# Kernel optimization log

Hardware: AMD Instinct MI355X
Metric: run time of the kernel (lower is better)

Reference implementation:

```python
import jax, jax.numpy as jnp
import numpy as np

D_MODEL = 1024
H = 16
D_K = D_MODEL // H
D_FF = 4096
EPS = 1e-6
NEG = -1e9


def layer_norm(x, alpha, beta):
    # Custom LN: scalar alpha/beta, unbiased std, eps added to std (not var)
    mean = jnp.mean(x, axis=-1, keepdims=True)
    std = jnp.std(x, axis=-1, ddof=1, keepdims=True)
    return alpha * (x - mean) / (std + EPS) + beta


def setup_inputs() -> dict:
    key = jax.random.key(0)
    ks = jax.random.split(key, 16)
    B, S = 4, 2048
    s = 1.0 / np.sqrt(D_MODEL)
    inp = {
        "x": jax.random.normal(ks[0], (B, S, D_MODEL), dtype=jnp.float32),
        "src_mask": jax.random.randint(ks[1], (B, 1, 1, S), 0, 2, dtype=jnp.int32),
        "wq": jax.random.normal(ks[2], (D_MODEL, D_MODEL), jnp.float32) * s,
        "bq": jnp.zeros((D_MODEL,), jnp.float32),
        "wk": jax.random.normal(ks[3], (D_MODEL, D_MODEL), jnp.float32) * s,
        "bk": jnp.zeros((D_MODEL,), jnp.float32),
        "wv": jax.random.normal(ks[4], (D_MODEL, D_MODEL), jnp.float32) * s,
        "bv": jnp.zeros((D_MODEL,), jnp.float32),
        "wo": jax.random.normal(ks[5], (D_MODEL, D_MODEL), jnp.float32) * s,
        "bo": jnp.zeros((D_MODEL,), jnp.float32),
        "w1": jax.random.normal(ks[6], (D_MODEL, D_FF), jnp.float32) * s,
        "b1": jnp.zeros((D_FF,), jnp.float32),
        "w2": jax.random.normal(ks[7], (D_FF, D_MODEL), jnp.float32) * (1.0 / np.sqrt(D_FF)),
        "b2": jnp.zeros((D_MODEL,), jnp.float32),
        "a1": jnp.ones((1,), jnp.float32),
        "be1": jnp.zeros((1,), jnp.float32),
        "a2": jnp.ones((1,), jnp.float32),
        "be2": jnp.zeros((1,), jnp.float32),
    }
    return inp


def reference(x, src_mask, wq, bq, wk, bk, wv, bv, wo, bo, w1, b1, w2, b2, a1, be1, a2, be2):
    B, S, _ = x.shape

    # --- residual 1: self-attention on pre-LN input (dropout = identity, eval) ---
    xn = layer_norm(x, a1, be1)
    q = (xn @ wq + bq).reshape(B, S, H, D_K).transpose(0, 2, 1, 3)  # [B,H,S,Dk]
    k = (xn @ wk + bk).reshape(B, S, H, D_K).transpose(0, 2, 1, 3)
    v = (xn @ wv + bv).reshape(B, S, H, D_K).transpose(0, 2, 1, 3)

    scores = jnp.einsum("bhqd,bhkd->bhqk", q, k) / jnp.sqrt(jnp.float32(D_K))
    scores = jnp.where(src_mask == 0, jnp.float32(NEG), scores)
    attn = jax.nn.softmax(scores, axis=-1)
    ctx = jnp.einsum("bhqk,bhkd->bhqd", attn, v)  # [B,H,S,Dk]
    ctx = ctx.transpose(0, 2, 1, 3).reshape(B, S, D_MODEL)
    attn_out = ctx @ wo + bo
    x = x + attn_out

    # --- residual 2: feed-forward on pre-LN input ---
    xn2 = layer_norm(x, a2, be2)
    ff = jax.nn.relu(xn2 @ w1 + b1) @ w2 + b2
    return x + ff
```

## Files before the change

### kernel.cpp

```cpp
#include <hip/hip_runtime.h>
#include <stdint.h>

typedef unsigned short u16;
typedef __attribute__((ext_vector_type(8))) short short8;
typedef __attribute__((ext_vector_type(4))) float f32x4;
typedef __attribute__((ext_vector_type(4))) u16 u16x4;
typedef __attribute__((ext_vector_type(4))) uint32_t u32x4;

#define NB 4
#define SEQ 2048
#define DM 1024
#define NH 16
#define DKh 64
#define DFF 4096
#define LOG2E 1.44269504089f

__device__ __forceinline__ u16 f2bf(float f) {
  union { float f; uint32_t u; } v; v.f = f;
  uint32_t u = v.u;
  return (u16)((u + 0x7FFFu + ((u >> 16) & 1u)) >> 16);
}

__device__ __forceinline__ uint32_t cvtpk(float lo, float hi) {
  uint32_t r;
  asm("v_cvt_pk_bf16_f32 %0, %1, %2" : "=v"(r) : "v"(lo), "v"(hi));
  return r;
}

__device__ __forceinline__ float fexp2(float x) {
  float r;
  asm("v_exp_f32 %0, %1" : "=v"(r) : "v"(x));
  return r;
}

__device__ __forceinline__ void gl16(const u16* g, u16* l) {
  __builtin_amdgcn_global_load_lds((const __attribute__((address_space(1))) void*)g,
                                   (__attribute__((address_space(3))) void*)l, 16, 0, 0);
}

__global__ __launch_bounds__(256) void transpose4_bf16(const float* __restrict__ s0,
                                                       const float* __restrict__ s1,
                                                       const float* __restrict__ s2,
                                                       const float* __restrict__ s3,
                                                       u16* __restrict__ d0,
                                                       u16* __restrict__ d1,
                                                       u16* __restrict__ d2,
                                                       u16* __restrict__ d3) {
  __shared__ float tile[32][33];
  int z = blockIdx.z;
  const float* src = (z == 0) ? s0 : (z == 1) ? s1 : (z == 2) ? s2 : s3;
  u16* dst = (z == 0) ? d0 : (z == 1) ? d1 : (z == 2) ? d2 : d3;
  int tx = threadIdx.x, ty = threadIdx.y;
  int c0 = blockIdx.x * 32, r0 = blockIdx.y * 32;
#pragma unroll
  for (int i = 0; i < 32; i += 8)
    tile[ty + i][tx] = src[(size_t)(r0 + ty + i) * DM + c0 + tx];
  __syncthreads();
#pragma unroll
  for (int i = 0; i < 32; i += 8)
    dst[(size_t)(c0 + ty + i) * DM + r0 + tx] = f2bf(tile[tx][ty + i]);
}

__global__ __launch_bounds__(256) void transpose_bf16(const float* __restrict__ src,
                                                      u16* __restrict__ dst, int R, int C) {
  __shared__ float tile[32][33];
  int tx = threadIdx.x, ty = threadIdx.y;
  int c0 = blockIdx.x * 32, r0 = blockIdx.y * 32;
#pragma unroll
  for (int i = 0; i < 32; i += 8)
    tile[ty + i][tx] = src[(size_t)(r0 + ty + i) * C + c0 + tx];
  __syncthreads();
#pragma unroll
  for (int i = 0; i < 32; i += 8)
    dst[(size_t)(c0 + ty + i) * R + r0 + tx] = f2bf(tile[tx][ty + i]);
}

__global__ __launch_bounds__(256) void bias_cat(const float* __restrict__ bq,
                                                const float* __restrict__ bk,
                                                const float* __restrict__ bv,
                                                float* __restrict__ o) {
  int i = blockIdx.x * 256 + threadIdx.x;
  if (i < 3072) o[i] = (i < 1024) ? bq[i] : ((i < 2048) ? bk[i - 1024] : bv[i - 2048]);
}

__global__ __launch_bounds__(1024) void compact_idx(const int* __restrict__ msk,
                                                    int* __restrict__ pinv,
                                                    int* __restrict__ lArr,
                                                    int* __restrict__ lpArr,
                                                    float* __restrict__ fbbc) {
  int b = blockIdx.x;
  int t = threadIdx.x;
  int lane = t & 63, w = t >> 6;
  int i0 = t * 2, i1 = t * 2 + 1;
  int m0 = msk[b * SEQ + i0] ? 1 : 0;
  int m1 = msk[b * SEQ + i1] ? 1 : 0;
  int s = m0 + m1;
  int run = s;
#pragma unroll
  for (int d = 1; d < 64; d <<= 1) {
    int v = __shfl_up(run, d);
    if (lane >= d) run += v;
  }
  __shared__ int wtot[16];
  __shared__ int woff[17];
  if (lane == 63) wtot[w] = run;
  __syncthreads();
  if (t == 0) {
    int acc = 0;
#pragma unroll
    for (int i = 0; i < 16; ++i) { woff[i] = acc; acc += wtot[i]; }
    woff[16] = acc;
  }
  __syncthreads();
  int excl = run - s + woff[w];
  pinv[b * SEQ + i0] = m0 ? excl : -1;
  pinv[b * SEQ + i1] = m1 ? (excl + m0) : -1;
  int L = woff[16];
  if (t == 0) {
    lArr[b] = L;
    int LP = (L + 63) & ~63;
    if (LP == 0) LP = 64;
    lpArr[b] = LP;
  }
  for (int l = t; l < SEQ; l += 1024)
    fbbc[b * SEQ + l] = (l < L) ? 0.0f : -1e9f;
}

__global__ __launch_bounds__(256) void ln_bf16(const float* __restrict__ x,
                                               u16* __restrict__ out,
                                               const float* __restrict__ alpha,
                                               const float* __restrict__ beta) {
  int row = blockIdx.x;
  const float4* xr = (const float4*)(x + (size_t)row * DM);
  int t = threadIdx.x;
  float4 v = xr[t];
  float s = v.x + v.y + v.z + v.w;
  float s2 = v.x * v.x + v.y * v.y + v.z * v.z + v.w * v.w;
#pragma unroll
  for (int m = 1; m < 64; m <<= 1) { s += __shfl_xor(s, m); s2 += __shfl_xor(s2, m); }
  __shared__ float red[8];
  int wid = t >> 6, lane = t & 63;
  if (lane == 0) { red[wid] = s; red[wid + 4] = s2; }
  __syncthreads();
  float S = red[0] + red[1] + red[2] + red[3];
  float S2 = red[4] + red[5] + red[6] + red[7];
  float mean = S * (1.0f / DM);
  float var = fmaxf((S2 - S * mean) * (1.0f / (DM - 1)), 0.0f);
  float inv = alpha[0] / (sqrtf(var) + 1e-6f);
  float bet = beta[0];
  u16x4 o;
  o[0] = f2bf((v.x - mean) * inv + bet);
  o[1] = f2bf((v.y - mean) * inv + bet);
  o[2] = f2bf((v.z - mean) * inv + bet);
  o[3] = f2bf((v.w - mean) * inv + bet);
  *(u16x4*)(out + (size_t)row * DM + t * 4) = o;
}

template <int MODE>
__global__ __launch_bounds__(512, 1) void gemm256(const u16* __restrict__ A,
                                                  const u16* __restrict__ WT,
                                                  const float* __restrict__ bias,
                                                  u16* __restrict__ outp,
                                                  const int* __restrict__ pinv,
                                                  int M, int N, int K, float qscale) {
  extern __shared__ u16 lds[];
  int tid = threadIdx.x;
  int lane = tid & 63, wid = tid >> 6;
  int lr = lane & 15, lg = lane >> 4;
  int wr = wid >> 2, wc = wid & 3;
  int nbx = N >> 8;
  int nwg = (M >> 8) * nbx;
  int lid = blockIdx.x;
  int swz = (lid & 7) * (nwg >> 3) + (lid >> 3);
  int m0 = (swz / nbx) << 8, n0 = (swz % nbx) << 8;

  int rowih = wid * 16 + (lane >> 2);
  int cchunk = lane & 3;
  int csrc = cchunk ^ ((rowih >> 1) & 3);
  size_t a_src = (size_t)(m0 + rowih) * K + csrc * 8;
  size_t b_src = (size_t)(n0 + rowih) * K + csrc * 8;
  u16* a_dst = lds + rowih * 32 + cchunk * 8;
  u16* b_dst = a_dst + 8192;

#define STAGE_A(B_, T_) do { \
    const u16* s_ = A + a_src + (size_t)(T_) * 32; \
    gl16(s_, a_dst + (B_) * 16384); \
    gl16(s_ + (size_t)128 * K, a_dst + (B_) * 16384 + 4096); \
  } while (0)
#define STAGE_B(B_, T_) do { \
    const u16* s_ = WT + b_src + (size_t)(T_) * 32; \
    gl16(s_, b_dst + (B_) * 16384); \
    gl16(s_ + (size_t)128 * K, b_dst + (B_) * 16384 + 4096); \
  } while (0)

  int rchunk = (lg ^ ((lr >> 1) & 3)) * 8;
  int offA[8], offB[4];
#pragma unroll
  for (int i = 0; i < 8; ++i) offA[i] = (wr * 128 + i * 16 + lr) * 32 + rchunk;
#pragma unroll
  for (int j = 0; j < 4; ++j) offB[j] = (wc * 64 + j * 16 + lr) * 32 + rchunk;

  f32x4 acc[8][4] = {};

  int NT = K >> 5;
  STAGE_A(0, 0); STAGE_B(0, 0);
  STAGE_A(1, 1); STAGE_B(1, 1);
  asm volatile("s_waitcnt vmcnt(4)" ::: "memory");
  __builtin_amdgcn_s_barrier();

  int buf = 0;
  for (int t = 0; t < NT; ++t) {
    const u16* la = lds + buf * 16384;
    const u16* lb = la + 8192;
    int b2 = buf - 1; if (b2 < 0) b2 += 3;
    short8 af0[4], bfr[4];
#pragma unroll
    for (int i = 0; i < 4; ++i) af0[i] = *(const short8*)&la[offA[i]];
#pragma unroll
    for (int j = 0; j < 4; ++j) bfr[j] = *(const short8*)&lb[offB[j]];
    if (t + 2 < NT) STAGE_A(b2, t + 2);
    __builtin_amdgcn_s_setprio(1);
#pragma unroll
    for (int i = 0; i < 4; ++i)
#pragma unroll
      for (int j = 0; j < 4; ++j)
        acc[i][j] = __builtin_amdgcn_mfma_f32_16x16x32_bf16(af0[i], bfr[j], acc[i][j], 0, 0, 0);
    __builtin_amdgcn_s_setprio(0);
    short8 af1[4];
#pragma unroll
    for (int i = 0; i < 4; ++i) af1[i] = *(const short8*)&la[offA[i + 4]];
    if (t + 2 < NT) STAGE_B(b2, t + 2);
    if (t < NT - 2) asm volatile("s_waitcnt vmcnt(4)" ::: "memory");
    else            asm volatile("s_waitcnt vmcnt(0)" ::: "memory");
    __builtin_amdgcn_s_setprio(1);
#pragma unroll
    for (int i = 0; i < 4; ++i)
#pragma unroll
      for (int j = 0; j < 4; ++j)
        acc[i + 4][j] = __builtin_amdgcn_mfma_f32_16x16x32_bf16(af1[i], bfr[j], acc[i + 4][j], 0, 0, 0);
    __builtin_amdgcn_s_setprio(0);
    __builtin_amdgcn_s_barrier();
    __builtin_amdgcn_sched_barrier(0);
    buf = (buf == 2) ? 0 : buf + 1;
  }
#undef STAGE_A
#undef STAGE_B

#pragma unroll
  for (int i = 0; i < 8; ++i) {
#pragma unroll
    for (int j = 0; j < 4; ++j) {
      int col = n0 + wc * 64 + j * 16 + lr;
      float bi = bias[col];
      int rbase = m0 + wr * 128 + i * 16 + lg * 4;
      if (MODE == 0) {
        int which = col >> 10, nc = col & 1023;
        int hh = nc >> 6, dd = nc & 63;
        int bb = rbase >> 11, ss = rbase & 2047;
        if (which == 0) {
          u16* dst = outp;
#pragma unroll
          for (int r = 0; r < 4; ++r)
            dst[((size_t)(bb * NH + hh) * SEQ + (ss + r)) * DKh + dd] = f2bf((acc[i][j][r] + bi) * qscale);
        } else {
          int4 p4 = *(const int4*)(pinv + bb * SEQ + ss);
          int pos[4] = {p4.x, p4.y, p4.z, p4.w};
          if (which == 1) {
            u16* kcb = outp + (size_t)(8u << 20);
#pragma unroll
            for (int r = 0; r < 4; ++r)
              if (pos[r] >= 0)
                kcb[((size_t)(bb * NH + hh) * SEQ + pos[r]) * DKh + dd] = f2bf(acc[i][j][r] + bi);
          } else {
            u16* vcb = outp + (size_t)2 * (8u << 20);
#pragma unroll
            for (int r = 0; r < 4; ++r)
              if (pos[r] >= 0) {
                int l = pos[r];
                int lo = l & 63;
                int pi = ((lo >> 4) & 1) * 32 + ((lo >> 2) & 3) * 8 + (lo >> 5) * 4 + (lo & 3);
                vcb[((size_t)(bb * NH + hh) * DKh + dd) * SEQ + (l & ~63) + pi] = f2bf(acc[i][j][r] + bi);
              }
          }
        }
      } else {
#pragma unroll
        for (int r = 0; r < 4; ++r)
          outp[(size_t)(rbase + r) * N + col] = f2bf(fmaxf(acc[i][j][r] + bi, 0.0f));
      }
    }
  }
}

__global__ __launch_bounds__(512, 4) void gemm_v2(const u16* __restrict__ A,
                                                  const u16* __restrict__ WT,
                                                  const float* __restrict__ bias,
                                                  const float* __restrict__ resid,
                                                  float* __restrict__ outp,
                                                  int M, int N, int K) {
  extern __shared__ u16 lds[];
  int tid = threadIdx.x;
  int lane = tid & 63, wid = tid >> 6;
  int lr = lane & 15, lg = lane >> 4;
  int wr = wid >> 1, wc = wid & 1;
  int nbx = N >> 7;
  int nwg = (M >> 8) * nbx;
  int lid = blockIdx.x;
  int swz = (lid & 7) * (nwg >> 3) + (lid >> 3);
  int m0 = (swz / nbx) << 8, n0 = (swz % nbx) << 7;

  int sr = tid >> 2;
  int sch = tid & 3;
  int scs = sch ^ ((sr >> 1) & 3);
  size_t a_src = (size_t)(m0 + sr) * K + scs * 8;
  size_t b_src = (size_t)(n0 + sr) * K + scs * 8;
  u16* a_dst = lds + sr * 32 + sch * 8;
  u16* b_dst = lds + 8192 + sr * 32 + sch * 8;

#define STAGE(B_, T_) do { \
    gl16(A + a_src + (size_t)(T_) * 32, a_dst + (B_) * 12288); \
    gl16(A + a_src + (size_t)128 * K + (size_t)(T_) * 32, a_dst + (B_) * 12288 + 4096); \
    gl16(WT + b_src + (size_t)(T_) * 32, b_dst + (B_) * 12288); \
  } while (0)

  int rchunk = (lg ^ ((lr >> 1) & 3)) * 8;
  int offA[4], offB[4];
#pragma unroll
  for (int i = 0; i < 4; ++i) offA[i] = (wr * 64 + i * 16 + lr) * 32 + rchunk;
#pragma unroll
  for (int j = 0; j < 4; ++j) offB[j] = 8192 + (wc * 64 + j * 16 + lr) * 32 + rchunk;

  f32x4 acc[4][4] = {};

  int NT = K >> 5;
  STAGE(0, 0);
  STAGE(1, 1);
  asm volatile("s_waitcnt vmcnt(3)" ::: "memory");
  __builtin_amdgcn_s_barrier();

  int buf = 0;
  for (int t = 0; t < NT; ++t) {
    const u16* la = lds + buf * 12288;
    int b2 = buf - 1; if (b2 < 0) b2 += 3;
    short8 af[4], bfr[4];
#pragma unroll
    for (int i = 0; i < 4; ++i) af[i] = *(const short8*)&la[offA[i]];
#pragma unroll
    for (int j = 0; j < 4; ++j) bfr[j] = *(const short8*)&la[offB[j]];
    if (t + 2 < NT) STAGE(b2, t + 2);
    __builtin_amdgcn_s_setprio(1);
#pragma unroll
    for (int i = 0; i < 4; ++i)
#pragma unroll
      for (int j = 0; j < 4; ++j)
        acc[i][j] = __builtin_amdgcn_mfma_f32_16x16x32_bf16(af[i], bfr[j], acc[i][j], 0, 0, 0);
    __builtin_amdgcn_s_setprio(0);
    if (t < NT - 2) asm volatile("s_waitcnt vmcnt(3)" ::: "memory");
    else            asm volatile("s_waitcnt vmcnt(0)" ::: "memory");
    __builtin_amdgcn_s_barrier();
    __builtin_amdgcn_sched_barrier(0);
    buf = (buf == 2) ? 0 : buf + 1;
  }
#undef STAGE

#pragma unroll
  for (int i = 0; i < 4; ++i) {
#pragma unroll
    for (int j = 0; j < 4; ++j) {
      int col = n0 + wc * 64 + j * 16 + lr;
      float bi = bias[col];
      int rbase = m0 + wr * 64 + i * 16 + lg * 4;
#pragma unroll
      for (int r = 0; r < 4; ++r) {
        size_t idx = (size_t)(rbase + r) * N + col;
        outp[idx] = resid[idx] + acc[i][j][r] + bi;
      }
    }
  }
}

__global__ __launch_bounds__(256) void attn_fwd(const u16* __restrict__ q,
                                                const u16* __restrict__ kc,
                                                const u16* __restrict__ vc,
                                                const int* __restrict__ lArr,
                                                const int* __restrict__ lpArr,
                                                const float* __restrict__ fbbc,
                                                u16* __restrict__ ctx) {
  __shared__ u16 lds[2][8192];
  int tid = threadIdx.x;
  int wid = tid >> 6, lane = tid & 63;
  int lr = lane & 15, lg = lane >> 4;
  int bh = blockIdx.x;
  int b = bh >> 4, hh = bh & 15;
  int q0 = blockIdx.y * 128;
  const u16* qbase = q + (size_t)bh * SEQ * DKh;
  const u16* kcb = kc + (size_t)bh * SEQ * DKh;
  const u16* vcb = vc + (size_t)bh * DKh * SEQ;
  const float* fbbase = fbbc + b * SEQ;
  int Lb = lArr[b];
  int LP = lpArr[b];

  short8 qf[2][2];
#pragma unroll
  for (int i = 0; i < 2; ++i)
#pragma unroll
    for (int kk = 0; kk < 2; ++kk)
      qf[i][kk] = *(const short8*)(qbase + (size_t)(q0 + wid * 32 + i * 16 + lr) * DKh + kk * 32 + lg * 8);

  int srow = tid >> 3;
  int schk = tid & 7;
  int ks0 = srow * 64 + ((schk ^ (srow & 7)) * 8);
  int vs0 = srow * SEQ + ((schk ^ (srow & 7)) * 8);
  int dst0 = tid * 8;

#define STAGE(B_, KV0) do { \
    gl16(kcb + (size_t)(KV0) * 64 + ks0, &lds[B_][dst0]); \
    gl16(kcb + (size_t)(KV0) * 64 + ks0 + 2048, &lds[B_][dst0 + 2048]); \
    gl16(vcb + (size_t)(KV0) + vs0, &lds[B_][dst0 + 4096]); \
    gl16(vcb + (size_t)(KV0) + vs0 + 32 * SEQ, &lds[B_][dst0 + 6144]); \
  } while (0)

  int swzc = (lr & 7) << 3;

  f32x4 ot[2][4] = {};
  float mrow[2] = {-3e38f, -3e38f};
  float lsum[2] = {0.0f, 0.0f};

  STAGE(0, 0);
  __syncthreads();

  int buf = 0;
  for (int kv0 = 0; kv0 < LP; kv0 += 64) {
    if (kv0 + 64 < LP) STAGE(buf ^ 1, kv0 + 64);
    const u16* Ks = lds[buf];
    const u16* Vs = lds[buf] + 4096;

    f32x4 st[2][4] = {};
    __builtin_amdgcn_s_setprio(1);
#pragma unroll
    for (int kk = 0; kk < 2; ++kk) {
      short8 kf[4];
#pragma unroll
      for (int j = 0; j < 4; ++j)
        kf[j] = *(const short8*)&Ks[(j * 16 + lr) * 64 + ((kk * 32 + lg * 8) ^ swzc)];
#pragma unroll
      for (int i = 0; i < 2; ++i)
#pragma unroll
        for (int j = 0; j < 4; ++j)
          st[i][j] = __builtin_amdgcn_mfma_f32_16x16x32_bf16(kf[j], qf[i][kk], st[i][j], 0, 0, 0);
    }
    __builtin_amdgcn_s_setprio(0);

    bool tail = (kv0 + 64 > Lb);

    u32x4 pa[2][2];
#pragma unroll
    for (int i = 0; i < 2; ++i) {
      float p[4][4];
      if (tail) {
#pragma unroll
        for (int j = 0; j < 4; ++j) {
          float4 f4 = *(const float4*)(fbbase + kv0 + j * 16 + lg * 4);
          p[j][0] = st[i][j][0] + f4.x;
          p[j][1] = st[i][j][1] + f4.y;
          p[j][2] = st[i][j][2] + f4.z;
          p[j][3] = st[i][j][3] + f4.w;
        }
      } else {
#pragma unroll
        for (int j = 0; j < 4; ++j)
#pragma unroll
          for (int r = 0; r < 4; ++r) p[j][r] = st[i][j][r];
      }
      float mx = -3e38f;
#pragma unroll
      for (int j = 0; j < 4; ++j)
#pragma unroll
        for (int r = 0; r < 4; ++r) mx = fmaxf(mx, p[j][r]);
      mx = fmaxf(mx, __shfl_xor(mx, 16));
      mx = fmaxf(mx, __shfl_xor(mx, 32));
      float mnew = fmaxf(mrow[i], mx);
      if (!__all(mnew - mrow[i] <= 8.0f)) {
        float corr = fexp2(mrow[i] - mnew);
        lsum[i] *= corr;
#pragma unroll
        for (int jd = 0; jd < 4; ++jd)
#pragma unroll
          for (int r = 0; r < 4; ++r) ot[i][jd][r] *= corr;
        mrow[i] = mnew;
      }
      float ps = 0.0f;
#pragma unroll
      for (int j = 0; j < 4; ++j)
#pragma unroll
        for (int r = 0; r < 4; ++r) {
          float pv = fexp2(p[j][r] - mrow[i]);
          p[j][r] = pv;
          ps += pv;
        }
      ps += __shfl_xor(ps, 16);
      ps += __shfl_xor(ps, 32);
      lsum[i] += ps;
#pragma unroll
      for (int ks = 0; ks < 2; ++ks) {
        pa[i][ks][0] = cvtpk(p[ks][0], p[ks][1]);
        pa[i][ks][1] = cvtpk(p[ks][2], p[ks][3]);
        pa[i][ks][2] = cvtpk(p[ks + 2][0], p[ks + 2][1]);
        pa[i][ks][3] = cvtpk(p[ks + 2][2], p[ks + 2][3]);
      }
    }

    __builtin_amdgcn_s_setprio(1);
#pragma unroll
    for (int ks = 0; ks < 2; ++ks) {
      short8 vf[4];
#pragma unroll
      for (int jd = 0; jd < 4; ++jd)
        vf[jd] = *(const short8*)&Vs[(jd * 16 + lr) * 64 + ((ks * 32 + lg * 8) ^ swzc)];
#pragma unroll
      for (int i = 0; i < 2; ++i)
#pragma unroll
        for (int jd = 0; jd < 4; ++jd)
          ot[i][jd] = __builtin_amdgcn_mfma_f32_16x16x32_bf16(vf[jd], *(short8*)&pa[i][ks], ot[i][jd], 0, 0, 0);
    }
    __builtin_amdgcn_s_setprio(0);
    __syncthreads();
    buf ^= 1;
  }
#undef STAGE

  float inv0 = 1.0f / lsum[0], inv1 = 1.0f / lsum[1];
  u16* ep = &lds[0][wid * 2048];
#pragma unroll
  for (int i = 0; i < 2; ++i) {
    float inv = i ? inv1 : inv0;
#pragma unroll
    for (int jd = 0; jd < 4; ++jd) {
      uint32_t w0 = cvtpk(ot[i][jd][0] * inv, ot[i][jd][1] * inv);
      uint32_t w1 = cvtpk(ot[i][jd][2] * inv, ot[i][jd][3] * inv);
      uint32_t pk2[2] = {w0, w1};
      *(u16x4*)&ep[(i * 16 + lr) * 64 + ((jd * 16 + lg * 4) ^ swzc)] = *(u16x4*)pk2;
    }
  }
  __syncthreads();
  int q_ = lane >> 1;
  size_t orow = ((size_t)b * SEQ + q0 + wid * 32 + q_) * DM + hh * DKh;
#pragma unroll
  for (int it = 0; it < 4; ++it) {
    int dc = (lane & 1) * 32 + it * 8;
    short8 vv = *(const short8*)&ep[q_ * 64 + (dc ^ ((q_ & 7) << 3))];
    *(short8*)(ctx + orow + dc) = vv;
  }
}

extern "C" void kernel_launch(void* const* d_in, const int* in_sizes, int n_in,
                              void* d_out, int out_size, void* d_ws, size_t ws_size,
                              hipStream_t stream) {
  const float* x   = (const float*)d_in[0];
  const int*   msk = (const int*)d_in[1];
  const float* wq  = (const float*)d_in[2];
  const float* bq  = (const float*)d_in[3];
  const float* wk  = (const float*)d_in[4];
  const float* bk  = (const float*)d_in[5];
  const float* wv  = (const float*)d_in[6];
  const float* bv  = (const float*)d_in[7];
  const float* wo  = (const float*)d_in[8];
  const float* bo  = (const float*)d_in[9];
  const float* w1  = (const float*)d_in[10];
  const float* b1  = (const float*)d_in[11];
  const float* w2  = (const float*)d_in[12];
  const float* b2  = (const float*)d_in[13];
  const float* a1  = (const float*)d_in[14];
  const float* be1 = (const float*)d_in[15];
  const float* a2  = (const float*)d_in[16];
  const float* be2 = (const float*)d_in[17];
  float* out = (float*)d_out;

  u16* wqT = (u16*)d_ws;
  u16* wkT = wqT + (1u << 20);
  u16* wvT = wkT + (1u << 20);
  u16* woT = wvT + (1u << 20);
  u16* w1T = woT + (1u << 20);
  u16* w2T = w1T + (4u << 20);
  u16* xn  = w2T + (4u << 20);
  u16* qb  = xn  + (8u << 20);
  u16* kb  = qb  + (8u << 20);
  u16* vtb = kb  + (8u << 20);
  u16* ctx = vtb + (8u << 20);
  u16* hb  = qb;
  float* bcat = (float*)ctx;
  int*   pinv = (int*)(ctx + (8u << 20));
  int*   lArr = pinv + NB * SEQ;
  int*   lpArr = lArr + 16;
  float* fbbc = (float*)(lpArr + 16);

  (void)hipFuncSetAttribute((const void*)gemm256<0>, hipFuncAttributeMaxDynamicSharedMemorySize, 96 * 1024);
  (void)hipFuncSetAttribute((const void*)gemm256<3>, hipFuncAttributeMaxDynamicSharedMemorySize, 96 * 1024);
  (void)hipFuncSetAttribute((const void*)gemm_v2, hipFuncAttributeMaxDynamicSharedMemorySize, 72 * 1024);

  dim3 tb(32, 8);
  transpose4_bf16<<<dim3(32, 32, 4), tb, 0, stream>>>(wq, wk, wv, wo, wqT, wkT, wvT, woT);
  transpose_bf16<<<dim3(128, 32), tb, 0, stream>>>(w1, w1T, DM, DFF);
  transpose_bf16<<<dim3(32, 128), tb, 0, stream>>>(w2, w2T, DFF, DM);
  bias_cat<<<12, 256, 0, stream>>>(bq, bk, bv, bcat);
  compact_idx<<<NB, 1024, 0, stream>>>(msk, pinv, lArr, lpArr, fbbc);

  ln_bf16<<<NB * SEQ, 256, 0, stream>>>(x, xn, a1, be1);

  gemm256<0><<<384, 512, 96 * 1024, stream>>>(xn, wqT, bcat, qb, pinv, NB * SEQ, 3 * DM, DM, 0.125f * LOG2E);

  attn_fwd<<<dim3(NB * NH, SEQ / 128), 256, 0, stream>>>(qb, kb, vtb, lArr, lpArr, fbbc, ctx);

  gemm_v2<<<256, 512, 72 * 1024, stream>>>(ctx, woT, bo, x, out, NB * SEQ, DM, DM);

  ln_bf16<<<NB * SEQ, 256, 0, stream>>>(out, xn, a2, be2);

  gemm256<3><<<512, 512, 96 * 1024, stream>>>(xn, w1T, b1, hb, nullptr, NB * SEQ, DFF, DM, 1.0f);

  gemm_v2<<<256, 512, 72 * 1024, stream>>>(hb, w2T, b2, out, out, NB * SEQ, DM, DFF);
}
```

Before: 376.6 us.

## Restructure gemm256 main loop to BK=64 double-buffer with four-phase staged loads

Rewrites the 256x256 GEMM main loop to use a K-tile of 64 instead of 32, with two LDS buffers (128KB) in place of three 32-wide buffers. Each iteration is split into four MFMA quadrant phases, and each phase issues one quarter of the next tile's global-to-LDS loads. An 8-way XOR swizzle is used for the wider rows. The aim is to halve the number of loop iterations and barriers per K and to interleave loads with compute more evenly. In exchange it adds more barriers per iteration, prefetches only one tile ahead, and raises LDS usage.

Result: faster. 368.5 us (-2.1%).

```diff
diff --git a/kernel.cpp b/kernel.cpp
--- a/kernel.cpp
+++ b/kernel.cpp
@@ -174,77 +174,118 @@
   int swz = (lid & 7) * (nwg >> 3) + (lid >> 3);
   int m0 = (swz / nbx) << 8, n0 = (swz % nbx) << 8;
 
-  int rowih = wid * 16 + (lane >> 2);
-  int cchunk = lane & 3;
-  int csrc = cchunk ^ ((rowih >> 1) & 3);
-  size_t a_src = (size_t)(m0 + rowih) * K + csrc * 8;
-  size_t b_src = (size_t)(n0 + rowih) * K + csrc * 8;
-  u16* a_dst = lds + rowih * 32 + cchunk * 8;
-  u16* b_dst = a_dst + 8192;
-
-#define STAGE_A(B_, T_) do { \
-    const u16* s_ = A + a_src + (size_t)(T_) * 32; \
-    gl16(s_, a_dst + (B_) * 16384); \
-    gl16(s_ + (size_t)128 * K, a_dst + (B_) * 16384 + 4096); \
-  } while (0)
-#define STAGE_B(B_, T_) do { \
-    const u16* s_ = WT + b_src + (size_t)(T_) * 32; \
-    gl16(s_, b_dst + (B_) * 16384); \
-    gl16(s_ + (size_t)128 * K, b_dst + (B_) * 16384 + 4096); \
-  } while (0)
-
-  int rchunk = (lg ^ ((lr >> 1) & 3)) * 8;
-  int offA[8], offB[4];
-#pragma unroll
-  for (int i = 0; i < 8; ++i) offA[i] = (wr * 128 + i * 16 + lr) * 32 + rchunk;
-#pragma unroll
-  for (int j = 0; j < 4; ++j) offB[j] = (wc * 64 + j * 16 + lr) * 32 + rchunk;
+  int rsw = tid >> 3;
+  int csw = tid & 7;
+  int csrc8 = (csw ^ (rsw & 7)) * 8;
+  int b0row = (rsw & 31) + ((rsw >> 5) << 6);
+  size_t aS = (size_t)(m0 + rsw) * K + csrc8;
+  size_t bS = (size_t)(n0 + b0row) * K + csrc8;
+  u16* aD = lds + rsw * 64 + csw * 8;
+  u16* bD = lds + 16384 + b0row * 64 + csw * 8;
+
+#define SGA0(D_, T_) do { const u16* s_ = A + aS + (size_t)(T_) * 64; \
+    gl16(s_, aD + (D_) * 32768); gl16(s_ + (size_t)128 * K, aD + (D_) * 32768 + 8192); } while (0)
+#define SGA1(D_, T_) do { const u16* s_ = A + aS + (size_t)64 * K + (size_t)(T_) * 64; \
+    gl16(s_, aD + (D_) * 32768 + 4096); gl16(s_ + (size_t)128 * K, aD + (D_) * 32768 + 12288); } while (0)
+#define SGB0(D_, T_) do { const u16* s_ = WT + bS + (size_t)(T_) * 64; \
+    gl16(s_, bD + (D_) * 32768); gl16(s_ + (size_t)128 * K, bD + (D_) * 32768 + 8192); } while (0)
+#define SGB1(D_, T_) do { const u16* s_ = WT + bS + (size_t)32 * K + (size_t)(T_) * 64; \
+    gl16(s_, bD + (D_) * 32768 + 2048); gl16(s_ + (size_t)128 * K, bD + (D_) * 32768 + 10240); } while (0)
+
+  int xo = lr & 7;
+  int ck[2] = {((0 + lg) ^ xo) * 8, ((4 + lg) ^ xo) * 8};
+  int arow[8], brow[4];
+#pragma unroll
+  for (int i = 0; i < 8; ++i) arow[i] = (wr * 128 + i * 16 + lr) * 64;
+#pragma unroll
+  for (int j = 0; j < 4; ++j) brow[j] = 16384 + (wc * 64 + j * 16 + lr) * 64;
 
   f32x4 acc[8][4] = {};
-
-  int NT = K >> 5;
-  STAGE_A(0, 0); STAGE_B(0, 0);
-  STAGE_A(1, 1); STAGE_B(1, 1);
+  int NT = K >> 6;
+
+  SGA0(0, 0); SGB0(0, 0); SGB1(0, 0); SGA1(0, 0);
   asm volatile("s_waitcnt vmcnt(4)" ::: "memory");
   __builtin_amdgcn_s_barrier();
 
-  int buf = 0;
   for (int t = 0; t < NT; ++t) {
-    const u16* la = lds + buf * 16384;
-    const u16* lb = la + 8192;
-    int b2 = buf - 1; if (b2 < 0) b2 += 3;
-    short8 af0[4], bfr[4];
-#pragma unroll
-    for (int i = 0; i < 4; ++i) af0[i] = *(const short8*)&la[offA[i]];
-#pragma unroll
-    for (int j = 0; j < 4; ++j) bfr[j] = *(const short8*)&lb[offB[j]];
-    if (t + 2 < NT) STAGE_A(b2, t + 2);
+    const u16* la = lds + (t & 1) * 32768;
+    int dn = (t + 1) & 1;
+    int kn = t + 1;
+    bool st = (t + 1 < NT);
+    short8 a0[4][2], a1[4][2], b0[2][2], b1[2][2];
+
+#pragma unroll
+    for (int i = 0; i < 4; ++i) { a0[i][0] = *(const short8*)&la[arow[i] + ck[0]]; a0[i][1] = *(const short8*)&la[arow[i] + ck[1]]; }
+#pragma unroll
+    for (int j = 0; j < 2; ++j) { b0[j][0] = *(const short8*)&la[brow[j] + ck[0]]; b0[j][1] = *(const short8*)&la[brow[j] + ck[1]]; }
+    if (st) { SGA0(dn, kn); asm volatile("s_waitcnt vmcnt(4)" ::: "memory"); }
+    else    { asm volatile("s_waitcnt vmcnt(2)" ::: "memory"); }
+    __builtin_amdgcn_s_barrier();
     __builtin_amdgcn_s_setprio(1);
 #pragma unroll
     for (int i = 0; i < 4; ++i)
 #pragma unroll
-      for (int j = 0; j < 4; ++j)
-        acc[i][j] = __builtin_amdgcn_mfma_f32_16x16x32_bf16(af0[i], bfr[j], acc[i][j], 0, 0, 0);
+      for (int j = 0; j < 2; ++j) {
+        acc[i][j] = __builtin_amdgcn_mfma_f32_16x16x32_bf16(a0[i][0], b0[j][0], acc[i][j], 0, 0, 0);
+        acc[i][j] = __builtin_amdgcn_mfma_f32_16x16x32_bf16(a0[i][1], b0[j][1], acc[i][j], 0, 0, 0);
+      }
     __builtin_amdgcn_s_setprio(0);
-    short8 af1[4];
-#pragma unroll
-    for (int i = 0; i < 4; ++i) af1[i] = *(const short8*)&la[offA[i + 4]];
-    if (t + 2 < NT) STAGE_B(b2, t + 2);
-    if (t < NT - 2) asm volatile("s_waitcnt vmcnt(4)" ::: "memory");
-    else            asm volatile("s_waitcnt vmcnt(0)" ::: "memory");
+    __builtin_amdgcn_s_barrier();
+    __builtin_amdgcn_sched_barrier(0);
+
+#pragma unroll
+    for (int j = 0; j < 2; ++j) { b1[j][0] = *(const short8*)&la[brow[j + 2] + ck[0]]; b1[j][1] = *(const short8*)&la[brow[j + 2] + ck[1]]; }
+    if (st) { SGB0(dn, kn); asm volatile("s_waitcnt vmcnt(4)" ::: "memory"); }
+    else    { asm volatile("s_waitcnt vmcnt(0)" ::: "memory"); }
+    __builtin_amdgcn_s_barrier();
     __builtin_amdgcn_s_setprio(1);
 #pragma unroll
     for (int i = 0; i < 4; ++i)
 #pragma unroll
-      for (int j = 0; j < 4; ++j)
-        acc[i + 4][j] = __builtin_amdgcn_mfma_f32_16x16x32_bf16(af1[i], bfr[j], acc[i + 4][j], 0, 0, 0);
+      for (int j = 0; j < 2; ++j) {
+        acc[i][j + 2] = __builtin_amdgcn_mfma_f32_16x16x32_bf16(a0[i][0], b1[j][0], acc[i][j + 2], 0, 0, 0);
+        acc[i][j + 2] = __builtin_amdgcn_mfma_f32_16x16x32_bf16(a0[i][1], b1[j][1], acc[i][j + 2], 0, 0, 0);
+      }
     __builtin_amdgcn_s_setprio(0);
     __builtin_amdgcn_s_barrier();
     __builtin_amdgcn_sched_barrier(0);
-    buf = (buf == 2) ? 0 : buf + 1;
-  }
-#undef STAGE_A
-#undef STAGE_B
+
+#pragma unroll
+    for (int i = 0; i < 4; ++i) { a1[i][0] = *(const short8*)&la[arow[i + 4] + ck[0]]; a1[i][1] = *(const short8*)&la[arow[i + 4] + ck[1]]; }
+    if (st) SGB1(dn, kn);
+    __builtin_amdgcn_s_barrier();
+    __builtin_amdgcn_s_setprio(1);
+#pragma unroll
+    for (int i = 0; i < 4; ++i)
+#pragma unroll
+      for (int j = 0; j < 2; ++j) {
+        acc[i + 4][j + 2] = __builtin_amdgcn_mfma_f32_16x16x32_bf16(a1[i][0], b1[j][0], acc[i + 4][j + 2], 0, 0, 0);
+        acc[i + 4][j + 2] = __builtin_amdgcn_mfma_f32_16x16x32_bf16(a1[i][1], b1[j][1], acc[i + 4][j + 2], 0, 0, 0);
+      }
+    __builtin_amdgcn_s_setprio(0);
+    __builtin_amdgcn_s_barrier();
+    __builtin_amdgcn_sched_barrier(0);
+
+#pragma unroll
+    for (int j = 0; j < 2; ++j) { b0[j][0] = *(const short8*)&la[brow[j] + ck[0]]; b0[j][1] = *(const short8*)&la[brow[j] + ck[1]]; }
+    if (st) { SGA1(dn, kn); asm volatile("s_waitcnt vmcnt(4)" ::: "memory"); }
+    __builtin_amdgcn_s_barrier();
+    __builtin_amdgcn_s_setprio(1);
+#pragma unroll
+    for (int i = 0; i < 4; ++i)
+#pragma unroll
+      for (int j = 0; j < 2; ++j) {
+        acc[i + 4][j] = __builtin_amdgcn_mfma_f32_16x16x32_bf16(a1[i][0], b0[j][0], acc[i + 4][j], 0, 0, 0);
+        acc[i + 4][j] = __builtin_amdgcn_mfma_f32_16x16x32_bf16(a1[i][1], b0[j][1], acc[i + 4][j], 0, 0, 0);
+      }
+    __builtin_amdgcn_s_setprio(0);
+    __builtin_amdgcn_s_barrier();
+    __builtin_amdgcn_sched_barrier(0);
+  }
+#undef SGA0
+#undef SGA1
+#undef SGB0
+#undef SGB1
 
 #pragma unroll
   for (int i = 0; i < 8; ++i) {
@@ -594,8 +635,8 @@
   int*   lpArr = lArr + 16;
   float* fbbc = (float*)(lpArr + 16);
 
-  (void)hipFuncSetAttribute((const void*)gemm256<0>, hipFuncAttributeMaxDynamicSharedMemorySize, 96 * 1024);
-  (void)hipFuncSetAttribute((const void*)gemm256<3>, hipFuncAttributeMaxDynamicSharedMemorySize, 96 * 1024);
+  (void)hipFuncSetAttribute((const void*)gemm256<0>, hipFuncAttributeMaxDynamicSharedMemorySize, 128 * 1024);
+  (void)hipFuncSetAttribute((const void*)gemm256<3>, hipFuncAttributeMaxDynamicSharedMemorySize, 128 * 1024);
   (void)hipFuncSetAttribute((const void*)gemm_v2, hipFuncAttributeMaxDynamicSharedMemorySize, 72 * 1024);
 
   dim3 tb(32, 8);
@@ -607,7 +648,7 @@
 
   ln_bf16<<<NB * SEQ, 256, 0, stream>>>(x, xn, a1, be1);
 
-  gemm256<0><<<384, 512, 96 * 1024, stream>>>(xn, wqT, bcat, qb, pinv, NB * SEQ, 3 * DM, DM, 0.125f * LOG2E);
+  gemm256<0><<<384, 512, 128 * 1024, stream>>>(xn, wqT, bcat, qb, pinv, NB * SEQ, 3 * DM, DM, 0.125f * LOG2E);
 
   attn_fwd<<<dim3(NB * NH, SEQ / 128), 256, 0, stream>>>(qb, kb, vtb, lArr, lpArr, fbbc, ctx);
 
@@ -615,7 +656,7 @@
 
   ln_bf16<<<NB * SEQ, 256, 0, stream>>>(out, xn, a2, be2);
 
-  gemm256<3><<<512, 512, 96 * 1024, stream>>>(xn, w1T, b1, hb, nullptr, NB * SEQ, DFF, DM, 1.0f);
+  gemm256<3><<<512, 512, 128 * 1024, stream>>>(xn, w1T, b1, hb, nullptr, NB * SEQ, DFF, DM, 1.0f);
 
   gemm_v2<<<256, 512, 72 * 1024, stream>>>(hb, w2T, b2, out, out, NB * SEQ, DM, DFF);
 }
```
